# Kernel optimization log

Hardware: AMD Instinct MI355X
Metric: run time of the kernel (lower is better)

Reference implementation:

```python
import jax, jax.numpy as jnp
import numpy as np

RADIUS = 8.0   # matches init kwarg radius
EPS = 1e-8     # nn.CosineSimilarity eps


def _denorm(p, height, width):
    # kornia denormalize_pixel_coordinates: [-1,1] -> [0, size-1]
    scale = jnp.array([(width - 1) * 0.5, (height - 1) * 0.5], dtype=p.dtype)
    return (p + 1.0) * scale


def setup_inputs() -> dict:
    key = jax.random.key(0)
    k1, k2, k3, k4 = jax.random.split(key, 4)
    B, N, D = 4, 2048, 256
    features = jax.random.normal(k1, (B, N, D), dtype=jnp.float32)
    pts_src = jax.random.uniform(k2, (B, N, 2), dtype=jnp.float32) * 2.0 - 1.0
    pts_dst = jax.random.uniform(k3, (B, B, N, 2), dtype=jnp.float32) * 2.0 - 1.0
    invis_idx = jax.random.randint(k4, (3, 128), 0, N)
    return {"features": features, "pts_src": pts_src, "pts_dst": pts_dst,
            "invis_idx": invis_idx, "height": 480, "width": 640}


def reference(features, pts_src, pts_dst, invis_idx, height, width):
    # features: [B,N,D]; pts_src: [B,N,2]; pts_dst: [B,B,N,2]
    B, N, D = features.shape
    ps = _denorm(jax.lax.stop_gradient(pts_src), height, width)   # [B,N,2]
    pd = _denorm(jax.lax.stop_gradient(pts_dst), height, width)   # [B,B,N,2]

    # squared euclidean distance d2[i,j,n,m] = ||ps[i,n] - pd[i,j,m]||^2
    s_src = jnp.sum(ps * ps, axis=-1)          # [B,N]
    s_dst = jnp.sum(pd * pd, axis=-1)          # [B,B,N]
    cross = jnp.einsum('ind,ijmd->ijnm', ps, pd)
    d2 = s_src[:, None, :, None] + s_dst[:, :, None, :] - 2.0 * cross  # [B,B,N,N]
    mask = d2 <= RADIUS * RADIUS

    # pair p = i*B + j of the flattened [B^2] grid matches src batch j (p % B)
    # with dst batch i (p // B):
    # cos[i,j,n,m] = <features[j,n], features[i,m]> / max(|f_jn|*|f_im|, eps)
    dots = jnp.einsum('jnd,imd->ijnm', features, features)  # [B,B,N,N]
    norms = jnp.sqrt(jnp.sum(features * features, axis=-1))  # [B,N]
    denom = jnp.maximum(norms[None, :, :, None] * norms[:, None, None, :], EPS)
    cos = dots / denom

    cnt = jnp.maximum(jnp.sum(mask), 1).astype(features.dtype)
    return jnp.sum(jnp.where(mask, 1.0 - cos, 0.0)) / cnt
```

## Files before the change

kernel.cpp:

```cpp
#include <hip/hip_runtime.h>

#define BB 4
#define NN 2048
#define DD 256
#define GCX 40
#define GCY 30
#define NCELL (GCX * GCY)
#define CSTRIDE 1216
#define OCTW 5
#define STILE 256
#define NTIL (NN / STILE)
#define MBLK (BB * BB * NTIL * 8)
#define WQ_CAP 160

#define OFF_BX    131072
#define OFF_BM    (131072 + 262144)
#define OFF_PSUM  (131072 + 262144 + 131072)
#define OFF_PCNT  (OFF_PSUM + 4096)

__device__ __forceinline__ int cell_clamp(int v, int hi) {
    return v < 0 ? 0 : (v > hi ? hi : v);
}

__global__ __launch_bounds__(256) void build_kernel(const float* __restrict__ pts_dst,
                                                    const int* __restrict__ hptr,
                                                    const int* __restrict__ wptr,
                                                    int* __restrict__ starts,
                                                    float2* __restrict__ bx,
                                                    int* __restrict__ bm) {
    __shared__ int cnt[NCELL];
    __shared__ int tsum[256];
    const int pair = blockIdx.x;
    const float sx = ((float)(*wptr) - 1.0f) * 0.5f;
    const float sy = ((float)(*hptr) - 1.0f) * 0.5f;

    for (int t = threadIdx.x; t < NCELL; t += 256) cnt[t] = 0;
    __syncthreads();

    const float2* pd = (const float2*)(pts_dst + (size_t)pair * NN * 2);
    float qx[8], qy[8]; int qc[8];
#pragma unroll
    for (int k = 0; k < 8; ++k) {
        const float2 r = pd[threadIdx.x + k * 256];
        qx[k] = fmaf(r.x, sx, sx);
        qy[k] = fmaf(r.y, sy, sy);
        const int cx = cell_clamp((int)(qx[k] * 0.0625f), GCX - 1);
        const int cy = cell_clamp((int)(qy[k] * 0.0625f), GCY - 1);
        qc[k] = cx + GCX * cy;
        atomicAdd(&cnt[qc[k]], 1);
    }
    __syncthreads();

    const int base = threadIdx.x * 5;
    int loc[5]; int s = 0;
#pragma unroll
    for (int k = 0; k < 5; ++k) {
        const int c = base + k;
        const int v = (c < NCELL) ? cnt[c] : 0;
        loc[k] = s; s += v;
    }
    tsum[threadIdx.x] = s;
    __syncthreads();
    for (int off = 1; off < 256; off <<= 1) {
        const int v = (threadIdx.x >= off) ? tsum[threadIdx.x - off] : 0;
        __syncthreads();
        tsum[threadIdx.x] += v;
        __syncthreads();
    }
    const int tbase = tsum[threadIdx.x] - s;
    int* gst = starts + pair * CSTRIDE;
#pragma unroll
    for (int k = 0; k < 5; ++k) {
        const int c = base + k;
        if (c < NCELL) {
            const int st = tbase + loc[k];
            gst[c] = st;
            cnt[c] = st;
        }
    }
    if (threadIdx.x == 0) gst[NCELL] = NN;
    __syncthreads();

    float2* gbx = bx + (size_t)pair * NN;
    int*    gbm = bm + (size_t)pair * NN;
#pragma unroll
    for (int k = 0; k < 8; ++k) {
        const int pos = atomicAdd(&cnt[qc[k]], 1);
        gbx[pos] = make_float2(qx[k], qy[k]);
        gbm[pos] = threadIdx.x + k * 256;
    }
}

__global__ __launch_bounds__(256, 4) void match_kernel(const float* __restrict__ feat,
                                                       const float* __restrict__ pts_src,
                                                       const int* __restrict__ hptr,
                                                       const int* __restrict__ wptr,
                                                       const int* __restrict__ starts,
                                                       const float2* __restrict__ bx,
                                                       const int* __restrict__ bm,
                                                       float* __restrict__ psum,
                                                       unsigned int* __restrict__ pcnt) {
    __shared__ unsigned int wq[4][WQ_CAP];
    __shared__ unsigned int wqc[4];
    __shared__ float bsum[4];
    __shared__ unsigned int bcnt[4];

    const int xcd  = blockIdx.x & 7;
    const int slot = blockIdx.x >> 3;
    const int pair = (xcd << 1) | (slot >> 6);
    const int rest = slot & 63;
    const int tile = rest >> 3;
    const int oct  = rest & 7;
    const int i = pair >> 2;
    const int j = pair & 3;
    const float sx = ((float)(*wptr) - 1.0f) * 0.5f;
    const float sy = ((float)(*hptr) - 1.0f) * 0.5f;

    const int wave = threadIdx.x >> 6;
    const int lane = threadIdx.x & 63;
    if (lane == 0) wqc[wave] = 0u;

    const int nloc = threadIdx.x;
    const float2 r = ((const float2*)pts_src)[(size_t)i * NN + tile * STILE + nloc];
    const float px = fmaf(r.x, sx, sx);
    const float py = fmaf(r.y, sy, sy);
    const int cxs = cell_clamp((int)(px * 0.0625f), GCX - 1);
    const int cys = cell_clamp((int)(py * 0.0625f), GCY - 1);

    const int*    gst = starts + pair * CSTRIDE;
    const float2* gbx = bx + (size_t)pair * NN;
    const int*    gbm = bm + (size_t)pair * NN;

#pragma unroll
    for (int dy = -1; dy <= 1; ++dy) {
        const int cy2 = cys + dy;
        if ((unsigned)cy2 >= (unsigned)GCY) continue;
#pragma unroll
        for (int dx = -1; dx <= 1; ++dx) {
            const int cx2 = cxs + dx;
            if ((unsigned)(cx2 - oct * OCTW) >= (unsigned)OCTW) continue;
            const int c = cx2 + GCX * cy2;
            const int e = gst[c + 1];
            for (int idx = gst[c]; idx < e; ++idx) {
                const float2 q = gbx[idx];
                const float ax = px - q.x, ay = py - q.y;
                if (fmaf(ax, ax, ay * ay) <= 64.0f) {
                    const unsigned int s2 = atomicAdd(&wqc[wave], 1u);
                    if (s2 < WQ_CAP) wq[wave][s2] = ((unsigned int)nloc << 11) | (unsigned int)idx;
                }
            }
        }
    }

    const unsigned int hc = min(wqc[wave], (unsigned int)WQ_CAP);
    const int g = lane >> 3, sub = lane & 7;
    float lsum = 0.0f;
    for (unsigned int h0 = 0; h0 < hc; h0 += 8) {
        const unsigned int hid = h0 + (unsigned int)g;
        const bool valid = hid < hc;
        float dd = 0.0f, aa = 0.0f, bb = 0.0f;
        if (valid) {
            const unsigned int rec = wq[wave][hid];
            const int m = gbm[rec & 2047u];
            const int n = tile * STILE + (int)(rec >> 11);
            const float4* pa = (const float4*)(feat + (size_t)(j * NN + n) * DD);
            const float4* pb = (const float4*)(feat + (size_t)(i * NN + m) * DD);
#pragma unroll
            for (int t = 0; t < 8; ++t) {
                const float4 a = pa[t * 8 + sub];
                const float4 b = pb[t * 8 + sub];
                dd = fmaf(a.x, b.x, fmaf(a.y, b.y, fmaf(a.z, b.z, fmaf(a.w, b.w, dd))));
                aa = fmaf(a.x, a.x, fmaf(a.y, a.y, fmaf(a.z, a.z, fmaf(a.w, a.w, aa))));
                bb = fmaf(b.x, b.x, fmaf(b.y, b.y, fmaf(b.z, b.z, fmaf(b.w, b.w, bb))));
            }
        }
        dd += __shfl_xor(dd, 1, 64);  aa += __shfl_xor(aa, 1, 64);  bb += __shfl_xor(bb, 1, 64);
        dd += __shfl_xor(dd, 2, 64);  aa += __shfl_xor(aa, 2, 64);  bb += __shfl_xor(bb, 2, 64);
        dd += __shfl_xor(dd, 4, 64);  aa += __shfl_xor(aa, 4, 64);  bb += __shfl_xor(bb, 4, 64);
        if (valid && sub == 0) {
            const float p = aa * bb;
            float rr = rsqrtf(p);
            rr = rr * (1.5f - 0.5f * p * rr * rr);
            lsum += 1.0f - dd * rr;
        }
    }
#pragma unroll
    for (int off = 32; off >= 1; off >>= 1) lsum += __shfl_xor(lsum, off, 64);

    if (lane == 0) { bsum[wave] = lsum; bcnt[wave] = hc; }
    __syncthreads();
    if (threadIdx.x == 0) {
        psum[blockIdx.x] = bsum[0] + bsum[1] + bsum[2] + bsum[3];
        pcnt[blockIdx.x] = bcnt[0] + bcnt[1] + bcnt[2] + bcnt[3];
    }
}

__global__ __launch_bounds__(256) void finalize_kernel(const float* __restrict__ psum,
                                                       const unsigned int* __restrict__ pcnt,
                                                       float* __restrict__ out) {
    float s = 0.0f;
    float c = 0.0f;
    for (int t = threadIdx.x; t < MBLK; t += 256) {
        s += psum[t];
        c += (float)pcnt[t];
    }
#pragma unroll
    for (int off = 32; off >= 1; off >>= 1) {
        s += __shfl_xor(s, off, 64);
        c += __shfl_xor(c, off, 64);
    }
    __shared__ float ss[4], cc[4];
    const int wave = threadIdx.x >> 6;
    const int lane = threadIdx.x & 63;
    if (lane == 0) { ss[wave] = s; cc[wave] = c; }
    __syncthreads();
    if (threadIdx.x == 0) {
        const float S = ss[0] + ss[1] + ss[2] + ss[3];
        const float C = cc[0] + cc[1] + cc[2] + cc[3];
        out[0] = S / fmaxf(C, 1.0f);
    }
}

extern "C" void kernel_launch(void* const* d_in, const int* in_sizes, int n_in,
                              void* d_out, int out_size, void* d_ws, size_t ws_size,
                              hipStream_t stream) {
    const float* feat    = (const float*)d_in[0];
    const float* pts_src = (const float*)d_in[1];
    const float* pts_dst = (const float*)d_in[2];
    const int* hptr = (const int*)d_in[4];
    const int* wptr = (const int*)d_in[5];
    float* out = (float*)d_out;

    int*          starts = (int*)d_ws;
    float2*       bx     = (float2*)((char*)d_ws + OFF_BX);
    int*          bm     = (int*)((char*)d_ws + OFF_BM);
    float*        psum   = (float*)((char*)d_ws + OFF_PSUM);
    unsigned int* pcnt   = (unsigned int*)((char*)d_ws + OFF_PCNT);

    build_kernel<<<BB * BB, 256, 0, stream>>>(pts_dst, hptr, wptr, starts, bx, bm);
    match_kernel<<<MBLK, 256, 0, stream>>>(feat, pts_src, hptr, wptr,
                                           starts, bx, bm, psum, pcnt);
    finalize_kernel<<<1, 256, 0, stream>>>(psum, pcnt, out);
}
```

Measured before the change: 93.71 us.

## Split neighbour search and cosine evaluation into separate kernels via global hit list

Match kernel now only finds neighbour pairs, scanning each row's three adjacent cells as one contiguous range instead of octant-split per-cell loops. It compacts the hits into a per-pair global list via atomics. A new cos_kernel assigns one hit per 8 lanes across a fixed grid, balancing the feature dot-product work that was previously tied to each block's hit count. This adds a kernel launch and a global round trip for the hit list, and truncates silently if any pair exceeds HCAP hits.

```diff
diff --git a/kernel.cpp b/kernel.cpp
--- a/kernel.cpp
+++ b/kernel.cpp
@@ -3,20 +3,21 @@
 #define BB 4
 #define NN 2048
 #define DD 256
+#define NPAIR 16
 #define GCX 40
 #define GCY 30
 #define NCELL (GCX * GCY)
 #define CSTRIDE 1216
-#define OCTW 5
-#define STILE 256
-#define NTIL (NN / STILE)
-#define MBLK (BB * BB * NTIL * 8)
-#define WQ_CAP 160
-
-#define OFF_BX    131072
-#define OFF_BM    (131072 + 262144)
-#define OFF_PSUM  (131072 + 262144 + 131072)
-#define OFF_PCNT  (OFF_PSUM + 4096)
+#define HCAP 4096
+#define WQ_CAP 256
+#define MBLK (NPAIR * 8)
+#define CBLK (NPAIR * 128)
+
+#define OFF_BX 131072
+#define OFF_BM (OFF_BX + 262144)
+#define OFF_HC (OFF_BM + 131072)
+#define OFF_HL (OFF_HC + 4096)
+#define OFF_PS (OFF_HL + 262144)
 
 __device__ __forceinline__ int cell_clamp(int v, int hi) {
     return v < 0 ? 0 : (v > hi ? hi : v);
@@ -27,12 +28,14 @@
                                                     const int* __restrict__ wptr,
                                                     int* __restrict__ starts,
                                                     float2* __restrict__ bx,
-                                                    int* __restrict__ bm) {
+                                                    int* __restrict__ bm,
+                                                    unsigned int* __restrict__ hitcnt) {
     __shared__ int cnt[NCELL];
     __shared__ int tsum[256];
     const int pair = blockIdx.x;
     const float sx = ((float)(*wptr) - 1.0f) * 0.5f;
     const float sy = ((float)(*hptr) - 1.0f) * 0.5f;
+    if (threadIdx.x == 0) hitcnt[pair] = 0u;
 
     for (int t = threadIdx.x; t < NCELL; t += 256) cnt[t] = 0;
     __syncthreads();
@@ -91,28 +94,19 @@
     }
 }
 
-__global__ __launch_bounds__(256, 4) void match_kernel(const float* __restrict__ feat,
-                                                       const float* __restrict__ pts_src,
-                                                       const int* __restrict__ hptr,
-                                                       const int* __restrict__ wptr,
-                                                       const int* __restrict__ starts,
-                                                       const float2* __restrict__ bx,
-                                                       const int* __restrict__ bm,
-                                                       float* __restrict__ psum,
-                                                       unsigned int* __restrict__ pcnt) {
+__global__ __launch_bounds__(256) void match_kernel(const float* __restrict__ pts_src,
+                                                    const int* __restrict__ hptr,
+                                                    const int* __restrict__ wptr,
+                                                    const int* __restrict__ starts,
+                                                    const float2* __restrict__ bx,
+                                                    const int* __restrict__ bm,
+                                                    unsigned int* __restrict__ hitcnt,
+                                                    unsigned int* __restrict__ hitlist) {
     __shared__ unsigned int wq[4][WQ_CAP];
     __shared__ unsigned int wqc[4];
-    __shared__ float bsum[4];
-    __shared__ unsigned int bcnt[4];
-
-    const int xcd  = blockIdx.x & 7;
-    const int slot = blockIdx.x >> 3;
-    const int pair = (xcd << 1) | (slot >> 6);
-    const int rest = slot & 63;
-    const int tile = rest >> 3;
-    const int oct  = rest & 7;
+    const int pair = blockIdx.x & 15;
+    const int tile = blockIdx.x >> 4;
     const int i = pair >> 2;
-    const int j = pair & 3;
     const float sx = ((float)(*wptr) - 1.0f) * 0.5f;
     const float sy = ((float)(*hptr) - 1.0f) * 0.5f;
 
@@ -121,89 +115,107 @@
     if (lane == 0) wqc[wave] = 0u;
 
     const int nloc = threadIdx.x;
-    const float2 r = ((const float2*)pts_src)[(size_t)i * NN + tile * STILE + nloc];
+    const float2 r = ((const float2*)pts_src)[(size_t)i * NN + tile * 256 + nloc];
     const float px = fmaf(r.x, sx, sx);
     const float py = fmaf(r.y, sy, sy);
     const int cxs = cell_clamp((int)(px * 0.0625f), GCX - 1);
     const int cys = cell_clamp((int)(py * 0.0625f), GCY - 1);
+    const int cxlo = cxs > 0 ? cxs - 1 : 0;
+    const int cxhi = cxs < GCX - 1 ? cxs + 1 : GCX - 1;
 
     const int*    gst = starts + pair * CSTRIDE;
     const float2* gbx = bx + (size_t)pair * NN;
-    const int*    gbm = bm + (size_t)pair * NN;
 
 #pragma unroll
     for (int dy = -1; dy <= 1; ++dy) {
         const int cy2 = cys + dy;
         if ((unsigned)cy2 >= (unsigned)GCY) continue;
-#pragma unroll
-        for (int dx = -1; dx <= 1; ++dx) {
-            const int cx2 = cxs + dx;
-            if ((unsigned)(cx2 - oct * OCTW) >= (unsigned)OCTW) continue;
-            const int c = cx2 + GCX * cy2;
-            const int e = gst[c + 1];
-            for (int idx = gst[c]; idx < e; ++idx) {
-                const float2 q = gbx[idx];
-                const float ax = px - q.x, ay = py - q.y;
-                if (fmaf(ax, ax, ay * ay) <= 64.0f) {
-                    const unsigned int s2 = atomicAdd(&wqc[wave], 1u);
-                    if (s2 < WQ_CAP) wq[wave][s2] = ((unsigned int)nloc << 11) | (unsigned int)idx;
-                }
+        const int b0 = gst[cy2 * GCX + cxlo];
+        const int e0 = gst[cy2 * GCX + cxhi + 1];
+        for (int idx = b0; idx < e0; ++idx) {
+            const float2 q = gbx[idx];
+            const float ax = px - q.x, ay = py - q.y;
+            if (fmaf(ax, ax, ay * ay) <= 64.0f) {
+                const unsigned int s2 = atomicAdd(&wqc[wave], 1u);
+                if (s2 < WQ_CAP) wq[wave][s2] = ((unsigned int)nloc << 11) | (unsigned int)idx;
             }
         }
     }
 
-    const unsigned int hc = min(wqc[wave], (unsigned int)WQ_CAP);
-    const int g = lane >> 3, sub = lane & 7;
+    const unsigned int wn = min(wqc[wave], (unsigned int)WQ_CAP);
+    unsigned int wbase = 0u;
+    if (lane == 0) wbase = atomicAdd(&hitcnt[pair], wn);
+    wbase = (unsigned int)__shfl((int)wbase, 0, 64);
+    const int* gbm = bm + (size_t)pair * NN;
+    unsigned int* gl = hitlist + (size_t)pair * HCAP;
+    for (unsigned int t = lane; t < wn; t += 64) {
+        const unsigned int rec = wq[wave][t];
+        const int m = gbm[rec & 2047u];
+        const unsigned int n = (unsigned int)(tile * 256) + (rec >> 11);
+        const unsigned int pos = wbase + t;
+        if (pos < HCAP) gl[pos] = (n << 11) | (unsigned int)m;
+    }
+}
+
+__global__ __launch_bounds__(256, 4) void cos_kernel(const float* __restrict__ feat,
+                                                     const unsigned int* __restrict__ hitcnt,
+                                                     const unsigned int* __restrict__ hitlist,
+                                                     float* __restrict__ psum) {
+    __shared__ float bsum[4];
+    const int pair  = blockIdx.x & 15;
+    const int chunk = blockIdx.x >> 4;
+    const int i = pair >> 2;
+    const int j = pair & 3;
+    const int wave = threadIdx.x >> 6;
+    const int lane = threadIdx.x & 63;
+
+    const unsigned int cnt = min(hitcnt[pair], (unsigned int)HCAP);
+    const unsigned int hid = (unsigned int)(chunk * 32 + (threadIdx.x >> 3));
+    const int sub = threadIdx.x & 7;
+    const bool valid = hid < cnt;
+
+    float dd = 0.0f, aa = 0.0f, bb = 0.0f;
+    if (valid) {
+        const unsigned int rec = hitlist[(size_t)pair * HCAP + hid];
+        const int n = (int)(rec >> 11);
+        const int m = (int)(rec & 2047u);
+        const float4* pa = (const float4*)(feat + (size_t)(j * NN + n) * DD);
+        const float4* pb = (const float4*)(feat + (size_t)(i * NN + m) * DD);
+#pragma unroll
+        for (int t = 0; t < 8; ++t) {
+            const float4 a = pa[t * 8 + sub];
+            const float4 b = pb[t * 8 + sub];
+            dd = fmaf(a.x, b.x, fmaf(a.y, b.y, fmaf(a.z, b.z, fmaf(a.w, b.w, dd))));
+            aa = fmaf(a.x, a.x, fmaf(a.y, a.y, fmaf(a.z, a.z, fmaf(a.w, a.w, aa))));
+            bb = fmaf(b.x, b.x, fmaf(b.y, b.y, fmaf(b.z, b.z, fmaf(b.w, b.w, bb))));
+        }
+    }
+    dd += __shfl_xor(dd, 1, 64);  aa += __shfl_xor(aa, 1, 64);  bb += __shfl_xor(bb, 1, 64);
+    dd += __shfl_xor(dd, 2, 64);  aa += __shfl_xor(aa, 2, 64);  bb += __shfl_xor(bb, 2, 64);
+    dd += __shfl_xor(dd, 4, 64);  aa += __shfl_xor(aa, 4, 64);  bb += __shfl_xor(bb, 4, 64);
     float lsum = 0.0f;
-    for (unsigned int h0 = 0; h0 < hc; h0 += 8) {
-        const unsigned int hid = h0 + (unsigned int)g;
-        const bool valid = hid < hc;
-        float dd = 0.0f, aa = 0.0f, bb = 0.0f;
-        if (valid) {
-            const unsigned int rec = wq[wave][hid];
-            const int m = gbm[rec & 2047u];
-            const int n = tile * STILE + (int)(rec >> 11);
-            const float4* pa = (const float4*)(feat + (size_t)(j * NN + n) * DD);
-            const float4* pb = (const float4*)(feat + (size_t)(i * NN + m) * DD);
-#pragma unroll
-            for (int t = 0; t < 8; ++t) {
-                const float4 a = pa[t * 8 + sub];
-                const float4 b = pb[t * 8 + sub];
-                dd = fmaf(a.x, b.x, fmaf(a.y, b.y, fmaf(a.z, b.z, fmaf(a.w, b.w, dd))));
-                aa = fmaf(a.x, a.x, fmaf(a.y, a.y, fmaf(a.z, a.z, fmaf(a.w, a.w, aa))));
-                bb = fmaf(b.x, b.x, fmaf(b.y, b.y, fmaf(b.z, b.z, fmaf(b.w, b.w, bb))));
-            }
-        }
-        dd += __shfl_xor(dd, 1, 64);  aa += __shfl_xor(aa, 1, 64);  bb += __shfl_xor(bb, 1, 64);
-        dd += __shfl_xor(dd, 2, 64);  aa += __shfl_xor(aa, 2, 64);  bb += __shfl_xor(bb, 2, 64);
-        dd += __shfl_xor(dd, 4, 64);  aa += __shfl_xor(aa, 4, 64);  bb += __shfl_xor(bb, 4, 64);
-        if (valid && sub == 0) {
-            const float p = aa * bb;
-            float rr = rsqrtf(p);
-            rr = rr * (1.5f - 0.5f * p * rr * rr);
-            lsum += 1.0f - dd * rr;
-        }
+    if (valid && sub == 0) {
+        const float p = aa * bb;
+        float rr = rsqrtf(p);
+        rr = rr * (1.5f - 0.5f * p * rr * rr);
+        lsum = 1.0f - dd * rr;
     }
 #pragma unroll
     for (int off = 32; off >= 1; off >>= 1) lsum += __shfl_xor(lsum, off, 64);
 
-    if (lane == 0) { bsum[wave] = lsum; bcnt[wave] = hc; }
-    __syncthreads();
-    if (threadIdx.x == 0) {
+    if (lane == 0) bsum[wave] = lsum;
+    __syncthreads();
+    if (threadIdx.x == 0)
         psum[blockIdx.x] = bsum[0] + bsum[1] + bsum[2] + bsum[3];
-        pcnt[blockIdx.x] = bcnt[0] + bcnt[1] + bcnt[2] + bcnt[3];
-    }
 }
 
 __global__ __launch_bounds__(256) void finalize_kernel(const float* __restrict__ psum,
-                                                       const unsigned int* __restrict__ pcnt,
+                                                       const unsigned int* __restrict__ hitcnt,
                                                        float* __restrict__ out) {
     float s = 0.0f;
     float c = 0.0f;
-    for (int t = threadIdx.x; t < MBLK; t += 256) {
-        s += psum[t];
-        c += (float)pcnt[t];
-    }
+    for (int t = threadIdx.x; t < CBLK; t += 256) s += psum[t];
+    if (threadIdx.x < NPAIR) c = (float)hitcnt[threadIdx.x];
 #pragma unroll
     for (int off = 32; off >= 1; off >>= 1) {
         s += __shfl_xor(s, off, 64);
@@ -231,14 +243,16 @@
     const int* wptr = (const int*)d_in[5];
     float* out = (float*)d_out;
 
-    int*          starts = (int*)d_ws;
-    float2*       bx     = (float2*)((char*)d_ws + OFF_BX);
-    int*          bm     = (int*)((char*)d_ws + OFF_BM);
-    float*        psum   = (float*)((char*)d_ws + OFF_PSUM);
-    unsigned int* pcnt   = (unsigned int*)((char*)d_ws + OFF_PCNT);
-
-    build_kernel<<<BB * BB, 256, 0, stream>>>(pts_dst, hptr, wptr, starts, bx, bm);
-    match_kernel<<<MBLK, 256, 0, stream>>>(feat, pts_src, hptr, wptr,
-                                           starts, bx, bm, psum, pcnt);
-    finalize_kernel<<<1, 256, 0, stream>>>(psum, pcnt, out);
-}
+    int*          starts  = (int*)d_ws;
+    float2*       bx      = (float2*)((char*)d_ws + OFF_BX);
+    int*          bm      = (int*)((char*)d_ws + OFF_BM);
+    unsigned int* hitcnt  = (unsigned int*)((char*)d_ws + OFF_HC);
+    unsigned int* hitlist = (unsigned int*)((char*)d_ws + OFF_HL);
+    float*        psum    = (float*)((char*)d_ws + OFF_PS);
+
+    build_kernel<<<NPAIR, 256, 0, stream>>>(pts_dst, hptr, wptr, starts, bx, bm, hitcnt);
+    match_kernel<<<MBLK, 256, 0, stream>>>(pts_src, hptr, wptr, starts, bx, bm,
+                                           hitcnt, hitlist);
+    cos_kernel<<<CBLK, 256, 0, stream>>>(feat, hitcnt, hitlist, psum);
+    finalize_kernel<<<1, 256, 0, stream>>>(psum, hitcnt, out);
+}
```

Result: slower. 96.18 us (+2.6%).
